# Kernel optimization log

Hardware: AMD Instinct MI355X
Metric: run time of the kernel (lower is better)

## Reference

```python
import jax, jax.numpy as jnp
import numpy as np

B, S, D, H = 2, 2048, 1024, 16
HD = D // H  # head_dim = 64
ROPE_BASE = 10000.0


def _rope_tables(seq_len, head_dim, dtype):
    inv_freq = 1.0 / (ROPE_BASE ** (jnp.arange(0, head_dim, 2, dtype=jnp.float32) / head_dim))
    t = jnp.arange(seq_len, dtype=jnp.float32)
    freqs = jnp.outer(t, inv_freq)                      # [S, HD/2]
    emb = jnp.concatenate([freqs, freqs], axis=-1)      # [S, HD]
    return jnp.cos(emb).astype(dtype), jnp.sin(emb).astype(dtype)


def _rotate_half(x):
    x1, x2 = jnp.split(x, 2, axis=-1)
    return jnp.concatenate([-x2, x1], axis=-1)


def setup_inputs() -> dict:
    key = jax.random.key(0)
    k0, k1, k2, k3, k4 = jax.random.split(key, 5)
    std = 0.02
    return {
        "hidden_states": jax.random.normal(k0, (B, S, D), dtype=jnp.float32),
        "attention_mask": jnp.ones((B, S), dtype=jnp.int32),
        "Wq": jax.random.normal(k1, (D, D), dtype=jnp.float32) * std,
        "Wk": jax.random.normal(k2, (D, D), dtype=jnp.float32) * std,
        "Wv": jax.random.normal(k3, (D, D), dtype=jnp.float32) * std,
        "Wo": jax.random.normal(k4, (D, D), dtype=jnp.float32) * std,
    }


def reference(hidden_states, attention_mask, Wq, Wk, Wv, Wo):
    b, s, d = hidden_states.shape
    scale = HD ** -0.5

    # torch Linear (no bias): y = x @ W.T, then split heads -> [b, h, s, hd]
    def proj_heads(W):
        y = jnp.einsum('bsd,ed->bse', hidden_states, W)
        return y.reshape(b, s, H, HD).transpose(0, 2, 1, 3)

    q, k, v = proj_heads(Wq), proj_heads(Wk), proj_heads(Wv)

    cos, sin = _rope_tables(s, HD, q.dtype)   # [s, hd]
    cos, sin = cos[None, None], sin[None, None]
    q = q * cos + _rotate_half(q) * sin
    k = k * cos + _rotate_half(k) * sin

    attn = jnp.einsum('bhqd,bhkd->bhqk', q, k) * scale  # [b,h,s,s]
    # mask [b,s] broadcast over heads and query dim (matches expand in torch)
    attn = jnp.where(attention_mask[:, None, None, :] == 0, -jnp.inf, attn)
    attn = jax.nn.softmax(attn, axis=-1)

    out = jnp.einsum('bhqk,bhkd->bhqd', attn, v)
    out = out.transpose(0, 2, 1, 3).reshape(b, s, d)
    return jnp.einsum('bsd,ed->bse', out, Wo)
```

## Files before the change

kernel.cpp:

```cpp
#include <hip/hip_runtime.h>
#include <math.h>

#define B_  2
#define S_  2048
#define D_  1024
#define H_  16
#define HD_ 64
#define M_  (B_*S_)

typedef __attribute__((ext_vector_type(8)))  short s8v;
typedef __attribute__((ext_vector_type(4)))  int   i4v;
typedef __attribute__((ext_vector_type(4)))  float f4v;
typedef __attribute__((ext_vector_type(16))) float f16x;
#define MFMA16(a,b,c) __builtin_amdgcn_mfma_f32_16x16x32_bf16(a,b,c,0,0,0)
#define MFMA32(a,b,c) __builtin_amdgcn_mfma_f32_32x32x16_bf16(a,b,c,0,0,0)

typedef __attribute__((address_space(1))) const unsigned int uint_ga;
typedef __attribute__((address_space(3))) unsigned int       uint_ls;

__device__ __forceinline__ unsigned short f2bf(float x) {
    unsigned u = __float_as_uint(x);
    u += 0x7FFF + ((u >> 16) & 1);
    return (unsigned short)(u >> 16);
}
__device__ __forceinline__ void gld16(const unsigned short* g, short* l) {
    __builtin_amdgcn_global_load_lds((uint_ga*)g, (uint_ls*)l, 16, 0, 0);
}

#define SCALE2 0.1803368801111204f
#define MXF2   16.0f

__global__ __launch_bounds__(256) void cvt_bf16_kernel(
    const float* __restrict__ X,  const float* __restrict__ Wq,
    const float* __restrict__ Wk, const float* __restrict__ Wv,
    const float* __restrict__ Wo,
    unsigned short* __restrict__ Xb,  unsigned short* __restrict__ Wqb,
    unsigned short* __restrict__ Wkb, unsigned short* __restrict__ Wvb,
    unsigned short* __restrict__ Wob, float2* __restrict__ cst)
{
    int y = blockIdx.y;
    if (y == 5) {
        int i = blockIdx.x * 256 + threadIdx.x;
        if (i < S_ * 32) {
            int j = i >> 11, s = i & 2047;
            double inv = pow(10000.0, -(double)j / 32.0);
            double ang = (double)s * inv;
            cst[i] = make_float2((float)cos(ang), (float)sin(ang));
        }
        return;
    }
    const float* src = (y==0)?X:(y==1)?Wq:(y==2)?Wk:(y==3)?Wv:Wo;
    unsigned short* dst = (y==0)?Xb:(y==1)?Wqb:(y==2)?Wkb:(y==3)?Wvb:Wob;
    int n = (y==0) ? (M_*D_) : (D_*D_);
    int i = (blockIdx.x*256 + threadIdx.x)*4;
    if (i >= n) return;
    float4 v = *(const float4*)&src[i];
    ushort4 o;
    o.x = f2bf(v.x); o.y = f2bf(v.y); o.z = f2bf(v.z); o.w = f2bf(v.w);
    *(ushort4*)&dst[i] = o;
}

__device__ __forceinline__ void mfma_128x128(
    const unsigned short* __restrict__ Amat, const unsigned short* __restrict__ Bmat,
    int m0, int n0, short* As, short* Bs, f4v acc[4][4])
{
    int tid = threadIdx.x;
    int l = tid & 63, w = tid >> 6;
    int wm = w >> 1, wn = w & 1;
    int lm = l & 15, qd = l >> 4;
    int lm7 = lm & 7;

    f4v z = {0.f, 0.f, 0.f, 0.f};
#pragma unroll
    for (int mt = 0; mt < 4; mt++)
#pragma unroll
        for (int nt = 0; nt < 4; nt++) acc[mt][nt] = z;

    int rl = l >> 3;
    int kc = (l & 7) ^ rl;
    const unsigned short* aG = Amat + (size_t)(m0 + w*32 + rl) * D_ + kc*8;
    const unsigned short* bG = Bmat + (size_t)(n0 + w*32 + rl) * D_ + kc*8;
    short* aL = As + (w*32)*64;
    short* bL = Bs + (w*32)*64;

#pragma unroll 1
    for (int k0 = 0; k0 < D_; k0 += 64) {
        __syncthreads();
#pragma unroll
        for (int j = 0; j < 4; j++) {
            gld16(aG + k0 + (size_t)j*8*D_, aL + j*8*64);
            gld16(bG + k0 + (size_t)j*8*D_, bL + j*8*64);
        }
        __syncthreads();
#pragma unroll
        for (int half = 0; half < 2; half++) {
            int pc = (half*4 + qd) ^ lm7;
            s8v afr[4], bfr[4];
#pragma unroll
            for (int x = 0; x < 4; x++) {
                afr[x] = *(const s8v*)(As + ((wm*64 + x*16 + lm)*8 + pc)*8);
                bfr[x] = *(const s8v*)(Bs + ((wn*64 + x*16 + lm)*8 + pc)*8);
            }
#pragma unroll
            for (int mt = 0; mt < 4; mt++)
#pragma unroll
                for (int nt = 0; nt < 4; nt++)
                    acc[mt][nt] = MFMA16(afr[mt], bfr[nt], acc[mt][nt]);
        }
    }
}

__global__ __launch_bounds__(256, 2) void qkv_mfma_kernel(
    const unsigned short* __restrict__ Xb,
    const unsigned short* __restrict__ Wqb, const unsigned short* __restrict__ Wkb,
    const unsigned short* __restrict__ Wvb, const float2* __restrict__ cst,
    unsigned short* __restrict__ Q, unsigned short* __restrict__ K,
    unsigned short* __restrict__ Vt)
{
    __shared__ __align__(16) short As[8192], Bs[8192];
    int bx = blockIdx.x, by = blockIdx.y;
    int proj = by >> 3, f8 = by & 7;
    int l = threadIdx.x & 63, w = threadIdx.x >> 6;
    int wm = w >> 1, wn = w & 1, lm = l & 15, qd = l >> 4;

    f4v acc[4][4];
    if (proj < 2) {
        const unsigned short* Wm = proj ? Wkb : Wqb;
        mfma_128x128(Wm, Xb, f8*128, bx*128, As, Bs, acc);

        int b  = (bx*128) >> 11;
        int sb = ((bx*128) & 2047) + wn*64;
        int bh = b*H_ + f8*2 + wm;
        unsigned short* dst = proj ? K : Q;
        float post = proj ? 1.0f : SCALE2;
#pragma unroll
        for (int mt = 0; mt < 4; mt++) {
            float sgn = (mt < 2) ? -1.f : 1.f;
#pragma unroll
            for (int nt = 0; nt < 4; nt++) {
                int s = sb + nt*16 + lm;
                unsigned short ov[4];
#pragma unroll
                for (int r = 0; r < 4; r++) {
                    int d = mt*16 + qd*4 + r;
                    float2 cs = cst[(d & 31)*S_ + s];
                    float v = acc[mt][nt][r];
                    float p = acc[mt^2][nt][r];
                    ov[r] = f2bf((v*cs.x + sgn*p*cs.y) * post);
                }
                ushort4 ou; ou.x=ov[0]; ou.y=ov[1]; ou.z=ov[2]; ou.w=ov[3];
                *(ushort4*)&dst[((size_t)bh*S_ + s)*HD_ + mt*16 + qd*4] = ou;
            }
        }
    } else {
        mfma_128x128(Xb, Wvb, bx*128, f8*128, As, Bs, acc);

        int b  = (bx*128) >> 11;
        int sb = ((bx*128) & 2047) + wm*64;
        int bh = b*H_ + f8*2 + wn;
#pragma unroll
        for (int mt = 0; mt < 4; mt++)
#pragma unroll
            for (int nt = 0; nt < 4; nt++) {
                int dim = nt*16 + lm;
                int s   = sb + mt*16 + qd*4;
                ushort4 ou;
                ou.x = f2bf(acc[mt][nt][0]);
                ou.y = f2bf(acc[mt][nt][1]);
                ou.z = f2bf(acc[mt][nt][2]);
                ou.w = f2bf(acc[mt][nt][3]);
                *(ushort4*)&Vt[((size_t)bh*HD_ + dim)*S_ + s] = ou;
            }
    }
}

__global__ __launch_bounds__(256, 2) void flash_mfma_kernel(
    const unsigned short* __restrict__ Q, const unsigned short* __restrict__ K,
    const unsigned short* __restrict__ Vt, const int* __restrict__ mask,
    unsigned short* __restrict__ AO)
{
    __shared__ __align__(16) short Ksh[8192];
    __shared__ __align__(16) short Vsh[8192];
    __shared__ __align__(16) float msk[S_];

    int bh = blockIdx.y;
    int b = bh >> 4, h = bh & 15;
    int tid = threadIdx.x;
    int l = tid & 63, w = tid >> 6;
    int lq = l & 31;
    int hf = l >> 5;
    int q0 = blockIdx.x * 128 + w * 32;

    {
        int i0 = tid * 8;
        const int* mp = mask + b * S_ + i0;
#pragma unroll
        for (int jj = 0; jj < 8; jj++)
            msk[i0 + jj] = mp[jj] ? -MXF2 : -3.0e38f;
    }

    const unsigned short* Qr = Q + ((size_t)bh * S_ + q0 + lq) * HD_ + hf * 8;
    s8v qf[4];
#pragma unroll
    for (int dc = 0; dc < 4; dc++) qf[dc] = *(const s8v*)(Qr + dc * 16);

    f16x zz = {0.f};
    f16x oacc[2]; oacc[0] = zz; oacc[1] = zz;
    f16x lacc = zz;
    s8v ones;
#pragma unroll
    for (int j = 0; j < 8; j++) ones[j] = (short)0x3F80;

    const unsigned short* Kb = K  + (size_t)bh * S_ * HD_;
    const unsigned short* Vb = Vt + (size_t)bh * HD_ * S_;

    int fb0 = 2*w, fb1 = 2*w + 1;
    const unsigned short* kS0 = Kb + (size_t)((fb0>>2)*32 + lq) * HD_ + (fb0&3)*16 + hf*8;
    const unsigned short* kS1 = Kb + (size_t)((fb1>>2)*32 + lq) * HD_ + (fb1&3)*16 + hf*8;
    const unsigned short* vS0 = Vb + (size_t)((fb0>>2)*32 + lq) * S_  + (fb0&3)*16 + hf*8;
    const unsigned short* vS1 = Vb + (size_t)((fb1>>2)*32 + lq) * S_  + (fb1&3)*16 + hf*8;

    gld16(kS0, Ksh + fb0*512);
    gld16(kS1, Ksh + fb1*512);
    gld16(vS0, Vsh + fb0*512);
    gld16(vS1, Vsh + fb1*512);
    __syncthreads();

#pragma unroll 1
    for (int t = 0; t < S_ / 64; t++) {
        int buf  = (t & 1) * 4096;
        int nbuf = 4096 - buf;
        if (t < S_/64 - 1) {
            int koff = (t + 1) * 64;
            gld16(kS0 + (size_t)koff * HD_, Ksh + nbuf + fb0*512);
            gld16(kS1 + (size_t)koff * HD_, Ksh + nbuf + fb1*512);
            gld16(vS0 + koff,               Vsh + nbuf + fb0*512);
            gld16(vS1 + koff,               Vsh + nbuf + fb1*512);
        }

        f16x sa0 = zz, sa1 = zz;
#pragma unroll
        for (int dc = 0; dc < 4; dc++) {
            s8v kf0 = *(const s8v*)(Ksh + buf + (0*4 + dc)*512 + l*8);
            sa0 = MFMA32(kf0, qf[dc], sa0);
        }
#pragma unroll
        for (int dc = 0; dc < 4; dc++) {
            s8v kf1 = *(const s8v*)(Ksh + buf + (1*4 + dc)*512 + l*8);
            sa1 = MFMA32(kf1, qf[dc], sa1);
        }

        float p[32];
#pragma unroll
        for (int kt = 0; kt < 2; kt++)
#pragma unroll
            for (int g = 0; g < 4; g++) {
                f4v mv = *(const f4v*)&msk[t*64 + kt*32 + g*8 + hf*4];
#pragma unroll
                for (int i = 0; i < 4; i++) {
                    float raw = (kt == 0) ? sa0[g*4 + i] : sa1[g*4 + i];
                    p[kt*16 + g*4 + i] = exp2f(raw + mv[i]);
                }
            }
        int pk[16];
#pragma unroll
        for (int m = 0; m < 16; m++)
            pk[m] = __builtin_amdgcn_perm(__float_as_uint(p[2*m+1]),
                                          __float_as_uint(p[2*m]), 0x07060302);

#pragma unroll
        for (int kcc = 0; kcc < 4; kcc++) {
            int a = 4*kcc;
            int x01 = hf ? pk[a]   : pk[a+2];
            int x23 = hf ? pk[a+1] : pk[a+3];
            int y01 = __shfl_xor(x01, 32);
            int y23 = __shfl_xor(x23, 32);
            i4v fr;
            fr.x = hf ? y01 : pk[a];
            fr.y = hf ? y23 : pk[a+1];
            fr.z = hf ? pk[a+2] : y01;
            fr.w = hf ? pk[a+3] : y23;
            s8v pf = __builtin_bit_cast(s8v, fr);
#pragma unroll
            for (int dt = 0; dt < 2; dt++) {
                s8v vf = *(const s8v*)(Vsh + buf + (dt*4 + kcc)*512 + l*8);
                oacc[dt] = MFMA32(vf, pf, oacc[dt]);
            }
            lacc = MFMA32(ones, pf, lacc);
        }
        __syncthreads();
    }

    float invl = 1.0f / lacc[0];
    int qtok = q0 + lq;
    unsigned short* Or = AO + ((size_t)(b * S_ + qtok)) * D_ + h * HD_;
#pragma unroll
    for (int dt = 0; dt < 2; dt++)
#pragma unroll
        for (int g = 0; g < 4; g++) {
            int d0 = dt*32 + g*8 + hf*4;
            ushort4 o;
            o.x = f2bf(oacc[dt][g*4 + 0] * invl);
            o.y = f2bf(oacc[dt][g*4 + 1] * invl);
            o.z = f2bf(oacc[dt][g*4 + 2] * invl);
            o.w = f2bf(oacc[dt][g*4 + 3] * invl);
            *(ushort4*)&Or[d0] = o;
        }
}

__global__ __launch_bounds__(256, 2) void outproj_mfma_kernel(
    const unsigned short* __restrict__ AO, const unsigned short* __restrict__ Wob,
    float* __restrict__ out)
{
    __shared__ __align__(16) short As[8192], Bs[8192];
    int bx = blockIdx.x, by = blockIdx.y;
    int l = threadIdx.x & 63, w = threadIdx.x >> 6;
    int wm = w >> 1, wn = w & 1, lm = l & 15, qd = l >> 4;

    f4v acc[4][4];
    mfma_128x128(Wob, AO, by*128, bx*128, As, Bs, acc);

#pragma unroll
    for (int mt = 0; mt < 4; mt++)
#pragma unroll
        for (int nt = 0; nt < 4; nt++) {
            int tok = bx*128 + wn*64 + nt*16 + lm;
            int e   = by*128 + wm*64 + mt*16 + qd*4;
            *(f4v*)&out[(size_t)tok*D_ + e] = acc[mt][nt];
        }
}

extern "C" void kernel_launch(void* const* d_in, const int* in_sizes, int n_in,
                              void* d_out, int out_size, void* d_ws, size_t ws_size,
                              hipStream_t stream)
{
    const float* X    = (const float*)d_in[0];
    const int*   mask = (const int*)  d_in[1];
    const float* Wq   = (const float*)d_in[2];
    const float* Wk   = (const float*)d_in[3];
    const float* Wv   = (const float*)d_in[4];
    const float* Wo   = (const float*)d_in[5];
    float* out = (float*)d_out;

    unsigned short* ws = (unsigned short*)d_ws;
    unsigned short* Xb  = ws;
    unsigned short* Wqb = Xb  + (size_t)M_ * D_;
    unsigned short* Wkb = Wqb + (size_t)D_ * D_;
    unsigned short* Wvb = Wkb + (size_t)D_ * D_;
    unsigned short* Wob = Wvb + (size_t)D_ * D_;
    unsigned short* Qb  = Wob + (size_t)D_ * D_;
    unsigned short* Kb  = Qb  + (size_t)M_ * D_;
    unsigned short* Vtb = Kb  + (size_t)M_ * D_;
    unsigned short* AOb = Vtb + (size_t)M_ * D_;
    float2* cst = (float2*)(AOb + (size_t)M_ * D_);

    cvt_bf16_kernel<<<dim3(4096, 6), 256, 0, stream>>>(
        X, Wq, Wk, Wv, Wo, Xb, Wqb, Wkb, Wvb, Wob, cst);
    qkv_mfma_kernel<<<dim3(32, 24), 256, 0, stream>>>(
        Xb, Wqb, Wkb, Wvb, cst, Qb, Kb, Vtb);
    flash_mfma_kernel<<<dim3(S_ / 128, B_ * H_), 256, 0, stream>>>(
        Qb, Kb, Vtb, mask, AOb);
    outproj_mfma_kernel<<<dim3(32, 8), 256, 0, stream>>>(AOb, Wob, out);
}
```

Before: 208.5 us.

## Split flash attention key range across two wave groups with LDS reduction

Each flash block now runs 512 threads. Two groups of four waves each process half of the key sequence for the same 128 queries, and the partial outputs and row sums are merged through shared memory at the end. K/V staging moves from direct global-to-LDS loads to register prefetch followed by an LDS store. The mask bias now seeds the MFMA accumulator instead of being added after the product. The aim is to double the waves per block and halve each wave's serial loop to hide latency better, at the cost of the reduction step, extra syncs and possibly lower occupancy from register pressure under launch_bounds(512,4).

```diff
diff --git a/kernel.cpp b/kernel.cpp
--- a/kernel.cpp
+++ b/kernel.cpp
@@ -174,28 +174,29 @@
     }
 }
 
-__global__ __launch_bounds__(256, 2) void flash_mfma_kernel(
+__global__ __launch_bounds__(512, 4) void flash_mfma_kernel(
     const unsigned short* __restrict__ Q, const unsigned short* __restrict__ K,
     const unsigned short* __restrict__ Vt, const int* __restrict__ mask,
     unsigned short* __restrict__ AO)
 {
-    __shared__ __align__(16) short Ksh[8192];
-    __shared__ __align__(16) short Vsh[8192];
+    __shared__ __align__(16) short Ksh[2][2][4096];
+    __shared__ __align__(16) short Vsh[2][2][4096];
     __shared__ __align__(16) float msk[S_];
 
     int bh = blockIdx.y;
     int b = bh >> 4, h = bh & 15;
     int tid = threadIdx.x;
     int l = tid & 63, w = tid >> 6;
-    int lq = l & 31;
-    int hf = l >> 5;
-    int q0 = blockIdx.x * 128 + w * 32;
+    int hk = w >> 2;
+    int wq = w & 3;
+    int lq = l & 31, hf = l >> 5;
+    int q0 = blockIdx.x * 128 + wq * 32;
 
     {
-        int i0 = tid * 8;
+        int i0 = tid * 4;
         const int* mp = mask + b * S_ + i0;
 #pragma unroll
-        for (int jj = 0; jj < 8; jj++)
+        for (int jj = 0; jj < 4; jj++)
             msk[i0 + jj] = mp[jj] ? -MXF2 : -3.0e38f;
     }
 
@@ -211,57 +212,65 @@
 #pragma unroll
     for (int j = 0; j < 8; j++) ones[j] = (short)0x3F80;
 
-    const unsigned short* Kb = K  + (size_t)bh * S_ * HD_;
-    const unsigned short* Vb = Vt + (size_t)bh * HD_ * S_;
-
-    int fb0 = 2*w, fb1 = 2*w + 1;
+    const int KH = S_ / 2;
+    const unsigned short* Kb = K  + (size_t)bh * S_ * HD_ + (size_t)hk * KH * HD_;
+    const unsigned short* Vb = Vt + (size_t)bh * HD_ * S_ + hk * KH;
+
+    int fb0 = 2*wq, fb1 = 2*wq + 1;
     const unsigned short* kS0 = Kb + (size_t)((fb0>>2)*32 + lq) * HD_ + (fb0&3)*16 + hf*8;
     const unsigned short* kS1 = Kb + (size_t)((fb1>>2)*32 + lq) * HD_ + (fb1&3)*16 + hf*8;
     const unsigned short* vS0 = Vb + (size_t)((fb0>>2)*32 + lq) * S_  + (fb0&3)*16 + hf*8;
     const unsigned short* vS1 = Vb + (size_t)((fb1>>2)*32 + lq) * S_  + (fb1&3)*16 + hf*8;
 
-    gld16(kS0, Ksh + fb0*512);
-    gld16(kS1, Ksh + fb1*512);
-    gld16(vS0, Vsh + fb0*512);
-    gld16(vS1, Vsh + fb1*512);
-    __syncthreads();
+    s8v kr0 = *(const s8v*)(kS0);
+    s8v kr1 = *(const s8v*)(kS1);
+    s8v vr0 = *(const s8v*)(vS0);
+    s8v vr1 = *(const s8v*)(vS1);
+
+    int mbase0 = hk * KH;
 
 #pragma unroll 1
-    for (int t = 0; t < S_ / 64; t++) {
-        int buf  = (t & 1) * 4096;
-        int nbuf = 4096 - buf;
-        if (t < S_/64 - 1) {
+    for (int t = 0; t < KH / 64; t++) {
+        int buf = t & 1;
+        *(s8v*)(&Ksh[hk][buf][fb0*512 + l*8]) = kr0;
+        *(s8v*)(&Ksh[hk][buf][fb1*512 + l*8]) = kr1;
+        *(s8v*)(&Vsh[hk][buf][fb0*512 + l*8]) = vr0;
+        *(s8v*)(&Vsh[hk][buf][fb1*512 + l*8]) = vr1;
+        __syncthreads();
+        if (t < KH/64 - 1) {
             int koff = (t + 1) * 64;
-            gld16(kS0 + (size_t)koff * HD_, Ksh + nbuf + fb0*512);
-            gld16(kS1 + (size_t)koff * HD_, Ksh + nbuf + fb1*512);
-            gld16(vS0 + koff,               Vsh + nbuf + fb0*512);
-            gld16(vS1 + koff,               Vsh + nbuf + fb1*512);
-        }
-
-        f16x sa0 = zz, sa1 = zz;
+            kr0 = *(const s8v*)(kS0 + (size_t)koff * HD_);
+            kr1 = *(const s8v*)(kS1 + (size_t)koff * HD_);
+            vr0 = *(const s8v*)(vS0 + koff);
+            vr1 = *(const s8v*)(vS1 + koff);
+        }
+
+        int mb = mbase0 + t*64;
+        f16x sa0, sa1;
+#pragma unroll
+        for (int g = 0; g < 4; g++) {
+            f4v m0 = *(const f4v*)&msk[mb + g*8 + hf*4];
+            f4v m1 = *(const f4v*)&msk[mb + 32 + g*8 + hf*4];
+#pragma unroll
+            for (int i = 0; i < 4; i++) { sa0[g*4+i] = m0[i]; sa1[g*4+i] = m1[i]; }
+        }
 #pragma unroll
         for (int dc = 0; dc < 4; dc++) {
-            s8v kf0 = *(const s8v*)(Ksh + buf + (0*4 + dc)*512 + l*8);
+            s8v kf0 = *(const s8v*)(&Ksh[hk][buf][(0*4+dc)*512 + l*8]);
             sa0 = MFMA32(kf0, qf[dc], sa0);
         }
 #pragma unroll
         for (int dc = 0; dc < 4; dc++) {
-            s8v kf1 = *(const s8v*)(Ksh + buf + (1*4 + dc)*512 + l*8);
+            s8v kf1 = *(const s8v*)(&Ksh[hk][buf][(1*4+dc)*512 + l*8]);
             sa1 = MFMA32(kf1, qf[dc], sa1);
         }
 
         float p[32];
 #pragma unroll
-        for (int kt = 0; kt < 2; kt++)
-#pragma unroll
-            for (int g = 0; g < 4; g++) {
-                f4v mv = *(const f4v*)&msk[t*64 + kt*32 + g*8 + hf*4];
-#pragma unroll
-                for (int i = 0; i < 4; i++) {
-                    float raw = (kt == 0) ? sa0[g*4 + i] : sa1[g*4 + i];
-                    p[kt*16 + g*4 + i] = exp2f(raw + mv[i]);
-                }
-            }
+        for (int r = 0; r < 16; r++) p[r]      = exp2f(sa0[r]);
+#pragma unroll
+        for (int r = 0; r < 16; r++) p[16 + r] = exp2f(sa1[r]);
+
         int pk[16];
 #pragma unroll
         for (int m = 0; m < 16; m++)
@@ -283,29 +292,43 @@
             s8v pf = __builtin_bit_cast(s8v, fr);
 #pragma unroll
             for (int dt = 0; dt < 2; dt++) {
-                s8v vf = *(const s8v*)(Vsh + buf + (dt*4 + kcc)*512 + l*8);
+                s8v vf = *(const s8v*)(&Vsh[hk][buf][(dt*4+kcc)*512 + l*8]);
                 oacc[dt] = MFMA32(vf, pf, oacc[dt]);
             }
             lacc = MFMA32(ones, pf, lacc);
         }
-        __syncthreads();
-    }
-
-    float invl = 1.0f / lacc[0];
-    int qtok = q0 + lq;
-    unsigned short* Or = AO + ((size_t)(b * S_ + qtok)) * D_ + h * HD_;
-#pragma unroll
-    for (int dt = 0; dt < 2; dt++)
-#pragma unroll
-        for (int g = 0; g < 4; g++) {
-            int d0 = dt*32 + g*8 + hf*4;
-            ushort4 o;
-            o.x = f2bf(oacc[dt][g*4 + 0] * invl);
-            o.y = f2bf(oacc[dt][g*4 + 1] * invl);
-            o.z = f2bf(oacc[dt][g*4 + 2] * invl);
-            o.w = f2bf(oacc[dt][g*4 + 3] * invl);
-            *(ushort4*)&Or[d0] = o;
-        }
+    }
+
+    __syncthreads();
+    float* ob = (float*)&Ksh[0][0][0];
+    float* lb = msk;
+    int cidx = wq*64 + l;
+    if (hk == 1) {
+#pragma unroll
+        for (int dt = 0; dt < 2; dt++)
+#pragma unroll
+            for (int r = 0; r < 16; r++)
+                ob[(dt*16 + r)*256 + cidx] = oacc[dt][r];
+        lb[cidx] = lacc[0];
+    }
+    __syncthreads();
+    if (hk == 0) {
+        float invl = 1.0f / (lacc[0] + lb[cidx]);
+        int qtok = q0 + lq;
+        unsigned short* Or = AO + ((size_t)(b * S_ + qtok)) * D_ + h * HD_;
+#pragma unroll
+        for (int dt = 0; dt < 2; dt++)
+#pragma unroll
+            for (int g = 0; g < 4; g++) {
+                int d0 = dt*32 + g*8 + hf*4;
+                ushort4 o;
+                o.x = f2bf((oacc[dt][g*4+0] + ob[(dt*16+g*4+0)*256 + cidx]) * invl);
+                o.y = f2bf((oacc[dt][g*4+1] + ob[(dt*16+g*4+1)*256 + cidx]) * invl);
+                o.z = f2bf((oacc[dt][g*4+2] + ob[(dt*16+g*4+2)*256 + cidx]) * invl);
+                o.w = f2bf((oacc[dt][g*4+3] + ob[(dt*16+g*4+3)*256 + cidx]) * invl);
+                *(ushort4*)&Or[d0] = o;
+            }
+    }
 }
 
 __global__ __launch_bounds__(256, 2) void outproj_mfma_kernel(
@@ -358,7 +381,7 @@
         X, Wq, Wk, Wv, Wo, Xb, Wqb, Wkb, Wvb, Wob, cst);
     qkv_mfma_kernel<<<dim3(32, 24), 256, 0, stream>>>(
         Xb, Wqb, Wkb, Wvb, cst, Qb, Kb, Vtb);
-    flash_mfma_kernel<<<dim3(S_ / 128, B_ * H_), 256, 0, stream>>>(
+    flash_mfma_kernel<<<dim3(S_ / 128, B_ * H_), 512, 0, stream>>>(
         Qb, Kb, Vtb, mask, AOb);
     outproj_mfma_kernel<<<dim3(32, 8), 256, 0, stream>>>(AOb, Wob, out);
 }
```

New measurement: 245.8 us. 17.9% more time.

## Stage K/V tiles through registers and fold mask into MFMA accumulator init

Applied to the files above, without the earlier changes.

Replaces the direct global-to-LDS loads (gld16) with plain global loads into registers that are written to a double-buffered LDS tile at the top of each iteration. A single barrier per iteration now follows the store, replacing the trailing one. The mask bias is loaded into the QK^T accumulators before the MFMAs rather than added after them, which removes a separate add per score element. The register staging raises register pressure and adds explicit LDS writes, traded for letting the next tile's load overlap the current compute.

```diff
diff --git a/kernel.cpp b/kernel.cpp
--- a/kernel.cpp
+++ b/kernel.cpp
@@ -179,16 +179,15 @@
     const unsigned short* __restrict__ Vt, const int* __restrict__ mask,
     unsigned short* __restrict__ AO)
 {
-    __shared__ __align__(16) short Ksh[8192];
-    __shared__ __align__(16) short Vsh[8192];
+    __shared__ __align__(16) short Ksh[2][4096];
+    __shared__ __align__(16) short Vsh[2][4096];
     __shared__ __align__(16) float msk[S_];
 
     int bh = blockIdx.y;
     int b = bh >> 4, h = bh & 15;
     int tid = threadIdx.x;
     int l = tid & 63, w = tid >> 6;
-    int lq = l & 31;
-    int hf = l >> 5;
+    int lq = l & 31, hf = l >> 5;
     int q0 = blockIdx.x * 128 + w * 32;
 
     {
@@ -220,48 +219,53 @@
     const unsigned short* vS0 = Vb + (size_t)((fb0>>2)*32 + lq) * S_  + (fb0&3)*16 + hf*8;
     const unsigned short* vS1 = Vb + (size_t)((fb1>>2)*32 + lq) * S_  + (fb1&3)*16 + hf*8;
 
-    gld16(kS0, Ksh + fb0*512);
-    gld16(kS1, Ksh + fb1*512);
-    gld16(vS0, Vsh + fb0*512);
-    gld16(vS1, Vsh + fb1*512);
-    __syncthreads();
+    s8v kr0 = *(const s8v*)(kS0);
+    s8v kr1 = *(const s8v*)(kS1);
+    s8v vr0 = *(const s8v*)(vS0);
+    s8v vr1 = *(const s8v*)(vS1);
 
 #pragma unroll 1
     for (int t = 0; t < S_ / 64; t++) {
-        int buf  = (t & 1) * 4096;
-        int nbuf = 4096 - buf;
+        int buf = t & 1;
+        *(s8v*)(&Ksh[buf][fb0*512 + l*8]) = kr0;
+        *(s8v*)(&Ksh[buf][fb1*512 + l*8]) = kr1;
+        *(s8v*)(&Vsh[buf][fb0*512 + l*8]) = vr0;
+        *(s8v*)(&Vsh[buf][fb1*512 + l*8]) = vr1;
+        __syncthreads();
         if (t < S_/64 - 1) {
             int koff = (t + 1) * 64;
-            gld16(kS0 + (size_t)koff * HD_, Ksh + nbuf + fb0*512);
-            gld16(kS1 + (size_t)koff * HD_, Ksh + nbuf + fb1*512);
-            gld16(vS0 + koff,               Vsh + nbuf + fb0*512);
-            gld16(vS1 + koff,               Vsh + nbuf + fb1*512);
-        }
-
-        f16x sa0 = zz, sa1 = zz;
+            kr0 = *(const s8v*)(kS0 + (size_t)koff * HD_);
+            kr1 = *(const s8v*)(kS1 + (size_t)koff * HD_);
+            vr0 = *(const s8v*)(vS0 + koff);
+            vr1 = *(const s8v*)(vS1 + koff);
+        }
+
+        int mb = t * 64;
+        f16x sa0, sa1;
+#pragma unroll
+        for (int g = 0; g < 4; g++) {
+            f4v m0 = *(const f4v*)&msk[mb + g*8 + hf*4];
+            f4v m1 = *(const f4v*)&msk[mb + 32 + g*8 + hf*4];
+#pragma unroll
+            for (int i = 0; i < 4; i++) { sa0[g*4+i] = m0[i]; sa1[g*4+i] = m1[i]; }
+        }
 #pragma unroll
         for (int dc = 0; dc < 4; dc++) {
-            s8v kf0 = *(const s8v*)(Ksh + buf + (0*4 + dc)*512 + l*8);
+            s8v kf0 = *(const s8v*)(&Ksh[buf][(0*4+dc)*512 + l*8]);
             sa0 = MFMA32(kf0, qf[dc], sa0);
         }
 #pragma unroll
         for (int dc = 0; dc < 4; dc++) {
-            s8v kf1 = *(const s8v*)(Ksh + buf + (1*4 + dc)*512 + l*8);
+            s8v kf1 = *(const s8v*)(&Ksh[buf][(1*4+dc)*512 + l*8]);
             sa1 = MFMA32(kf1, qf[dc], sa1);
         }
 
         float p[32];
 #pragma unroll
-        for (int kt = 0; kt < 2; kt++)
-#pragma unroll
-            for (int g = 0; g < 4; g++) {
-                f4v mv = *(const f4v*)&msk[t*64 + kt*32 + g*8 + hf*4];
-#pragma unroll
-                for (int i = 0; i < 4; i++) {
-                    float raw = (kt == 0) ? sa0[g*4 + i] : sa1[g*4 + i];
-                    p[kt*16 + g*4 + i] = exp2f(raw + mv[i]);
-                }
-            }
+        for (int r = 0; r < 16; r++) p[r]      = exp2f(sa0[r]);
+#pragma unroll
+        for (int r = 0; r < 16; r++) p[16 + r] = exp2f(sa1[r]);
+
         int pk[16];
 #pragma unroll
         for (int m = 0; m < 16; m++)
@@ -283,12 +287,11 @@
             s8v pf = __builtin_bit_cast(s8v, fr);
 #pragma unroll
             for (int dt = 0; dt < 2; dt++) {
-                s8v vf = *(const s8v*)(Vsh + buf + (dt*4 + kcc)*512 + l*8);
+                s8v vf = *(const s8v*)(&Vsh[buf][(dt*4+kcc)*512 + l*8]);
                 oacc[dt] = MFMA32(vf, pf, oacc[dt]);
             }
             lacc = MFMA32(ones, pf, lacc);
         }
-        __syncthreads();
     }
 
     float invl = 1.0f / lacc[0];
```

Result: faster. 201.1 us (-3.6%).
